# Optimization experiments

Measured on AMD Instinct MI355X. Metric: run time of the kernel, lower is better.

Reference implementation:

```python
import jax, jax.numpy as jnp
import numpy as np

S, D = 8192, 2048      # sequence length, feature dim (input_size)
H, E, K, L = 64, 64, 2, 64  # gate hidden, expert count, top-k, expert layer_size
EPS = 1e-12            # torch F.normalize eps


def setup_inputs() -> dict:
    key = jax.random.key(0)
    ks = jax.random.split(key, 5)
    x = jax.random.normal(ks[0], (S, D), dtype=jnp.float32)
    # torch nn.Linear weights have shape [out_features, in_features]
    Wg_in = jax.random.normal(ks[1], (H, D), dtype=jnp.float32) * 0.02   # gate.input
    Wg_lin = jax.random.normal(ks[2], (E, H), dtype=jnp.float32) * 0.02  # gate.linear
    Wg_out = jax.random.normal(ks[3], (1, S), dtype=jnp.float32) * 0.02  # gate.output
    We = jax.random.normal(ks[4], (E, L, D), dtype=jnp.float32) * 0.02   # expert weight bank
    return {"x": x, "Wg_in": Wg_in, "Wg_lin": Wg_lin, "Wg_out": Wg_out, "We": We}


def reference(x, Wg_in, Wg_lin, Wg_out, We):
    # --- SparseGate (eval mode: dropout = identity) ---
    h = x @ Wg_in.T                         # [S, H]
    logits = h @ Wg_lin.T                   # [S, E]
    scores = (logits.T @ Wg_out.T)[:, 0]    # Linear(S,1) applied to [E,S] -> [E]
    topv, idx = jax.lax.top_k(scores, K)    # global top-k experts for whole input
    g = jax.nn.softmax(topv)                # softmax over the k selected logits

    # --- dispatch to k selected experts (FFNN: Linear -> normalize(-1) -> GELU) ---
    Wsel = We[idx]                          # [K, L, D]
    z = jnp.einsum('sd,kld->ksl', x, Wsel)  # [K, S, L]
    z = z / jnp.maximum(jnp.linalg.norm(z, axis=-1, keepdims=True), EPS)
    z = jax.nn.gelu(z, approximate=False)   # torch GELU default is exact erf

    # --- weighted combine: sum_k g_k * expert_k(x) ---
    return jnp.einsum('k,ksl->sl', g, z)    # [S, L]
```

## Files before the change

kernel.cpp:

```cpp
#include <hip/hip_runtime.h>
#include <hip/hip_bf16.h>
#include <math.h>

#define D_DIM 2048
#define L_DIM 64
#define E_NUM 64
#define H_DIM 64

typedef float f32x4_t __attribute__((ext_vector_type(4)));
typedef __bf16 bf16x8_t __attribute__((ext_vector_type(8)));

#define WS_UPART 0u
#define WS_U     (128u * 2048u * 4u)
#define WS_V     (WS_U + 2048u * 4u)
#define WS_META  (WS_V + 256u)
#define WS_WB    (WS_META + 64u)

__global__ void k_upart(const float* __restrict__ x, const float* __restrict__ wout,
                        float* __restrict__ upart) {
  const int d4 = (blockIdx.x * 256 + threadIdx.x) * 4;
  const int s0 = blockIdx.y * 64;
  const float* xp = x + (size_t)s0 * D_DIM + d4;
  float4 acc = make_float4(0.f, 0.f, 0.f, 0.f);
#pragma unroll 8
  for (int i = 0; i < 64; ++i) {
    const float w = wout[s0 + i];
    const float4 xv = *reinterpret_cast<const float4*>(xp + (size_t)i * D_DIM);
    acc.x += xv.x * w; acc.y += xv.y * w; acc.z += xv.z * w; acc.w += xv.w * w;
  }
  *reinterpret_cast<float4*>(upart + (size_t)blockIdx.y * D_DIM + d4) = acc;
}

__global__ void k_ufinish(const float* __restrict__ upart, float* __restrict__ u) {
  const int d = blockIdx.x * 256 + threadIdx.x;
  float s = 0.f;
#pragma unroll 8
  for (int c = 0; c < 128; ++c) s += upart[(size_t)c * D_DIM + d];
  u[d] = s;
}

__global__ void k_v(const float* __restrict__ wg_in, const float* __restrict__ u,
                    float* __restrict__ v) {
  const int h = blockIdx.x;
  const int t = threadIdx.x;
  const float4* wr = reinterpret_cast<const float4*>(wg_in + (size_t)h * D_DIM);
  const float4* ur = reinterpret_cast<const float4*>(u);
  float s = 0.f;
#pragma unroll
  for (int i = t; i < 512; i += 256) {
    const float4 a = wr[i];
    const float4 b = ur[i];
    s += a.x * b.x + a.y * b.y + a.z * b.z + a.w * b.w;
  }
  __shared__ float red[4];
#pragma unroll
  for (int off = 32; off; off >>= 1) s += __shfl_down(s, off, 64);
  if ((t & 63) == 0) red[t >> 6] = s;
  __syncthreads();
  if (t == 0) v[h] = red[0] + red[1] + red[2] + red[3];
}

__global__ void k_gate(const float* __restrict__ wg_lin, const float* __restrict__ v,
                       int* __restrict__ sel, float* __restrict__ g) {
  __shared__ float vv[H_DIM];
  __shared__ float sc[E_NUM];
  const int t = threadIdx.x;
  vv[t] = v[t];
  __syncthreads();
  float s = 0.f;
#pragma unroll 8
  for (int hh = 0; hh < H_DIM; ++hh) s += wg_lin[t * H_DIM + hh] * vv[hh];
  sc[t] = s;
  __syncthreads();
  if (t == 0) {
    int b1 = 0; float m1 = sc[0];
    for (int e = 1; e < E_NUM; ++e) { if (sc[e] > m1) { m1 = sc[e]; b1 = e; } }
    int b2 = -1; float m2 = -3.4e38f;
    for (int e = 0; e < E_NUM; ++e) {
      if (e != b1 && sc[e] > m2) { m2 = sc[e]; b2 = e; }
    }
    const float e2 = expf(m2 - m1);
    const float g0 = 1.0f / (1.0f + e2);
    sel[0] = b1; sel[1] = b2;
    g[0] = g0; g[1] = 1.0f - g0;
  }
}

__global__ void k_wb(const float* __restrict__ we, const int* __restrict__ sel,
                     __hip_bfloat16* __restrict__ wb) {
  const int n = blockIdx.x;
  const int e = sel[n >> 6];
  const int l = n & 63;
  const float* src = we + ((size_t)e * L_DIM + l) * D_DIM;
  const int t = threadIdx.x;
  const float4 a = reinterpret_cast<const float4*>(src)[2 * t];
  const float4 b = reinterpret_cast<const float4*>(src)[2 * t + 1];
  union { __hip_bfloat16 h[8]; uint4 u; } pk;
  pk.h[0] = __float2bfloat16(a.x); pk.h[1] = __float2bfloat16(a.y);
  pk.h[2] = __float2bfloat16(a.z); pk.h[3] = __float2bfloat16(a.w);
  pk.h[4] = __float2bfloat16(b.x); pk.h[5] = __float2bfloat16(b.y);
  pk.h[6] = __float2bfloat16(b.z); pk.h[7] = __float2bfloat16(b.w);
  reinterpret_cast<uint4*>(wb + (size_t)n * D_DIM)[t] = pk.u;
}

__device__ __forceinline__ void async_ld16(const void* gp, void* lp) {
  __builtin_amdgcn_global_load_lds(
      (const __attribute__((address_space(1))) unsigned int*)gp,
      (__attribute__((address_space(3))) unsigned int*)lp, 16, 0, 0);
}

__device__ __forceinline__ float gelu_f(float v) {
  return 0.5f * v * (1.0f + erff(v * 0.70710678118654752440f));
}

__global__ __launch_bounds__(256) void k_moe_gemm(
    const float* __restrict__ x, const __hip_bfloat16* __restrict__ wb,
    const float* __restrict__ gw, float* __restrict__ out) {
  __shared__ __align__(16) unsigned char lds[32 * 144 + 128 * 64 * 2];
  unsigned char* ldsA0 = lds;
  unsigned char* ldsB0 = lds + 32 * 144;

  const int tid = threadIdx.x;
  const int wv = tid >> 6;
  const int lane = tid & 63;
  const int m0 = blockIdx.x * 32;
  const float g0 = gw[0], g1 = gw[1];

  const int ar = tid >> 3, ac = tid & 7;
  const float* gA = x + (size_t)(m0 + ar) * D_DIM + ac * 8;
  unsigned char* ldsAw = ldsA0 + ar * 144 + ac * 16;

  const int fr = lane & 15, fq = lane >> 4;

  f32x4_t acc00 = {0.f, 0.f, 0.f, 0.f};
  f32x4_t acc01 = acc00, acc10 = acc00, acc11 = acc00;

  for (int kk = 0; kk < D_DIM / 64; ++kk) {
    const int k0 = kk * 64;
    if (kk) __syncthreads();
    const float4 a0 = *reinterpret_cast<const float4*>(gA + k0);
    const float4 a1 = *reinterpret_cast<const float4*>(gA + k0 + 4);
    union { __hip_bfloat16 h[8]; uint4 u; } pk;
    pk.h[0] = __float2bfloat16(a0.x); pk.h[1] = __float2bfloat16(a0.y);
    pk.h[2] = __float2bfloat16(a0.z); pk.h[3] = __float2bfloat16(a0.w);
    pk.h[4] = __float2bfloat16(a1.x); pk.h[5] = __float2bfloat16(a1.y);
    pk.h[6] = __float2bfloat16(a1.z); pk.h[7] = __float2bfloat16(a1.w);
    *reinterpret_cast<uint4*>(ldsAw) = pk.u;
#pragma unroll
    for (int i = 0; i < 4; ++i) {
      const int c = i * 256 + tid;
      const int r = c >> 3, p = c & 7;
      const int kc = p ^ (r & 7);
      async_ld16(wb + (size_t)r * D_DIM + k0 + kc * 8, ldsB0 + c * 16);
    }
    __syncthreads();
    union fragu { uint4 u; bf16x8_t v; };
    fragu af[2][2], bfr[2][2];
#pragma unroll
    for (int mt = 0; mt < 2; ++mt)
#pragma unroll
      for (int ks = 0; ks < 2; ++ks)
        af[mt][ks].u = *reinterpret_cast<const uint4*>(
            ldsA0 + (mt * 16 + fr) * 144 + ks * 64 + fq * 16);
#pragma unroll
    for (int nt = 0; nt < 2; ++nt)
#pragma unroll
      for (int ks = 0; ks < 2; ++ks) {
        const int r = wv * 32 + nt * 16 + fr;
        const int kg = ks * 4 + fq;
        bfr[nt][ks].u = *reinterpret_cast<const uint4*>(
            ldsB0 + r * 128 + ((kg ^ (r & 7)) * 16));
      }
    acc00 = __builtin_amdgcn_mfma_f32_16x16x32_bf16(af[0][0].v, bfr[0][0].v, acc00, 0, 0, 0);
    acc00 = __builtin_amdgcn_mfma_f32_16x16x32_bf16(af[0][1].v, bfr[0][1].v, acc00, 0, 0, 0);
    acc01 = __builtin_amdgcn_mfma_f32_16x16x32_bf16(af[0][0].v, bfr[1][0].v, acc01, 0, 0, 0);
    acc01 = __builtin_amdgcn_mfma_f32_16x16x32_bf16(af[0][1].v, bfr[1][1].v, acc01, 0, 0, 0);
    acc10 = __builtin_amdgcn_mfma_f32_16x16x32_bf16(af[1][0].v, bfr[0][0].v, acc10, 0, 0, 0);
    acc10 = __builtin_amdgcn_mfma_f32_16x16x32_bf16(af[1][1].v, bfr[0][1].v, acc10, 0, 0, 0);
    acc11 = __builtin_amdgcn_mfma_f32_16x16x32_bf16(af[1][0].v, bfr[1][0].v, acc11, 0, 0, 0);
    acc11 = __builtin_amdgcn_mfma_f32_16x16x32_bf16(af[1][1].v, bfr[1][1].v, acc11, 0, 0, 0);
  }
  __syncthreads();
  float* z = reinterpret_cast<float*>(lds);
  {
    const int colbase = wv * 32 + fr;
#pragma unroll
    for (int reg = 0; reg < 4; ++reg) {
      const int r0 = fq * 4 + reg;
      z[r0 * 132 + colbase]             = acc00[reg];
      z[r0 * 132 + colbase + 16]        = acc01[reg];
      z[(16 + r0) * 132 + colbase]      = acc10[reg];
      z[(16 + r0) * 132 + colbase + 16] = acc11[reg];
    }
  }
  __syncthreads();
  float* ps = reinterpret_cast<float*>(lds + 16896);
  {
    const int r = tid >> 3, seg = tid & 7;
    float s = 0.f;
#pragma unroll
    for (int i2 = 0; i2 < 16; ++i2) {
      const float t2 = z[r * 132 + seg * 16 + i2];
      s += t2 * t2;
    }
    ps[r * 8 + seg] = s;
  }
  __syncthreads();
  {
    const int r = tid >> 3, j = tid & 7;
    const float s0 = ps[r * 8 + 0] + ps[r * 8 + 1] + ps[r * 8 + 2] + ps[r * 8 + 3];
    const float s1 = ps[r * 8 + 4] + ps[r * 8 + 5] + ps[r * 8 + 6] + ps[r * 8 + 7];
    const float i0 = 1.0f / fmaxf(sqrtf(s0), 1e-12f);
    const float i1 = 1.0f / fmaxf(sqrtf(s1), 1e-12f);
    float o[8];
#pragma unroll
    for (int i2 = 0; i2 < 8; ++i2) {
      const int c = j * 8 + i2;
      const float za = z[r * 132 + c] * i0;
      const float zb = z[r * 132 + 64 + c] * i1;
      o[i2] = g0 * gelu_f(za) + g1 * gelu_f(zb);
    }
    float4* op = reinterpret_cast<float4*>(out + (size_t)(m0 + r) * 64 + j * 8);
    op[0] = make_float4(o[0], o[1], o[2], o[3]);
    op[1] = make_float4(o[4], o[5], o[6], o[7]);
  }
}

extern "C" void kernel_launch(void* const* d_in, const int* in_sizes, int n_in,
                              void* d_out, int out_size, void* d_ws, size_t ws_size,
                              hipStream_t stream) {
  (void)in_sizes; (void)n_in; (void)out_size; (void)ws_size;
  const float* x      = (const float*)d_in[0];
  const float* wg_in  = (const float*)d_in[1];
  const float* wg_lin = (const float*)d_in[2];
  const float* wg_out = (const float*)d_in[3];
  const float* we     = (const float*)d_in[4];
  float* out = (float*)d_out;
  char* ws = (char*)d_ws;

  float* upart = (float*)(ws + WS_UPART);
  float* u     = (float*)(ws + WS_U);
  float* v     = (float*)(ws + WS_V);
  int*   sel   = (int*)(ws + WS_META);
  float* g     = (float*)(ws + WS_META + 8);
  __hip_bfloat16* wb = (__hip_bfloat16*)(ws + WS_WB);

  k_upart  <<<dim3(2, 128), 256, 0, stream>>>(x, wg_out, upart);
  k_ufinish<<<8, 256, 0, stream>>>(upart, u);
  k_v      <<<64, 256, 0, stream>>>(wg_in, u, v);
  k_gate   <<<1, 64, 0, stream>>>(wg_lin, v, sel, g);
  k_wb     <<<128, 256, 0, stream>>>(we, sel, wb);
  k_moe_gemm<<<256, 256, 0, stream>>>(x, wb, g, out);
}
```

Measured before the change: 167.9 us.

## Fuse gate kernels, double-buffer MoE GEMM loads, halve row tile

The three small gate kernels (u finish, v projection, expert scoring/top-k) merge into one 1024-thread block, removing launches and global round-trips. k_upart now uses 128 rows per block with two accumulators, so there are half as many partials. The expert GEMM moves to 16-row tiles with 512 blocks and double-buffers both the async B loads and the A register prefetch, overlapping loads with MFMA. The tradeoffs are lower per-block MFMA reuse, serialized partial sums in a single block, and more register and LDS use.

New measurement: 170.8 us. No clear change (+1.7%).

```diff
diff --git a/kernel.cpp b/kernel.cpp
--- a/kernel.cpp
+++ b/kernel.cpp
@@ -11,74 +11,71 @@
 typedef __bf16 bf16x8_t __attribute__((ext_vector_type(8)));
 
 #define WS_UPART 0u
-#define WS_U     (128u * 2048u * 4u)
-#define WS_V     (WS_U + 2048u * 4u)
-#define WS_META  (WS_V + 256u)
+#define WS_META  (128u * 2048u * 4u + 2048u * 4u + 256u)
 #define WS_WB    (WS_META + 64u)
 
-__global__ void k_upart(const float* __restrict__ x, const float* __restrict__ wout,
-                        float* __restrict__ upart) {
+__global__ __launch_bounds__(256) void k_upart(const float* __restrict__ x,
+                                               const float* __restrict__ wout,
+                                               float* __restrict__ upart) {
   const int d4 = (blockIdx.x * 256 + threadIdx.x) * 4;
-  const int s0 = blockIdx.y * 64;
+  const int s0 = blockIdx.y * 128;
   const float* xp = x + (size_t)s0 * D_DIM + d4;
-  float4 acc = make_float4(0.f, 0.f, 0.f, 0.f);
+  float4 acc0 = make_float4(0.f, 0.f, 0.f, 0.f);
+  float4 acc1 = make_float4(0.f, 0.f, 0.f, 0.f);
 #pragma unroll 8
-  for (int i = 0; i < 64; ++i) {
-    const float w = wout[s0 + i];
-    const float4 xv = *reinterpret_cast<const float4*>(xp + (size_t)i * D_DIM);
-    acc.x += xv.x * w; acc.y += xv.y * w; acc.z += xv.z * w; acc.w += xv.w * w;
-  }
-  *reinterpret_cast<float4*>(upart + (size_t)blockIdx.y * D_DIM + d4) = acc;
-}
-
-__global__ void k_ufinish(const float* __restrict__ upart, float* __restrict__ u) {
-  const int d = blockIdx.x * 256 + threadIdx.x;
-  float s = 0.f;
+  for (int i = 0; i < 128; i += 2) {
+    const float w0 = wout[s0 + i];
+    const float w1 = wout[s0 + i + 1];
+    const float4 a = *reinterpret_cast<const float4*>(xp + (size_t)i * D_DIM);
+    const float4 b = *reinterpret_cast<const float4*>(xp + (size_t)(i + 1) * D_DIM);
+    acc0.x += a.x * w0; acc0.y += a.y * w0; acc0.z += a.z * w0; acc0.w += a.w * w0;
+    acc1.x += b.x * w1; acc1.y += b.y * w1; acc1.z += b.z * w1; acc1.w += b.w * w1;
+  }
+  acc0.x += acc1.x; acc0.y += acc1.y; acc0.z += acc1.z; acc0.w += acc1.w;
+  *reinterpret_cast<float4*>(upart + (size_t)blockIdx.y * D_DIM + d4) = acc0;
+}
+
+__global__ __launch_bounds__(1024) void k_gate_all(
+    const float* __restrict__ upart, const float* __restrict__ wg_in,
+    const float* __restrict__ wg_lin, int* __restrict__ sel, float* __restrict__ g) {
+  __shared__ float uS[D_DIM];
+  __shared__ float vS[H_DIM];
+  __shared__ float scS[E_NUM];
+  const int t = threadIdx.x;
+  for (int dd = t; dd < D_DIM; dd += 1024) {
+    float s = 0.f;
 #pragma unroll 8
-  for (int c = 0; c < 128; ++c) s += upart[(size_t)c * D_DIM + d];
-  u[d] = s;
-}
-
-__global__ void k_v(const float* __restrict__ wg_in, const float* __restrict__ u,
-                    float* __restrict__ v) {
-  const int h = blockIdx.x;
-  const int t = threadIdx.x;
-  const float4* wr = reinterpret_cast<const float4*>(wg_in + (size_t)h * D_DIM);
-  const float4* ur = reinterpret_cast<const float4*>(u);
-  float s = 0.f;
-#pragma unroll
-  for (int i = t; i < 512; i += 256) {
-    const float4 a = wr[i];
-    const float4 b = ur[i];
-    s += a.x * b.x + a.y * b.y + a.z * b.z + a.w * b.w;
-  }
-  __shared__ float red[4];
-#pragma unroll
-  for (int off = 32; off; off >>= 1) s += __shfl_down(s, off, 64);
-  if ((t & 63) == 0) red[t >> 6] = s;
-  __syncthreads();
-  if (t == 0) v[h] = red[0] + red[1] + red[2] + red[3];
-}
-
-__global__ void k_gate(const float* __restrict__ wg_lin, const float* __restrict__ v,
-                       int* __restrict__ sel, float* __restrict__ g) {
-  __shared__ float vv[H_DIM];
-  __shared__ float sc[E_NUM];
-  const int t = threadIdx.x;
-  vv[t] = v[t];
-  __syncthreads();
-  float s = 0.f;
+    for (int c = 0; c < 64; ++c) s += upart[(size_t)c * D_DIM + dd];
+    uS[dd] = s;
+  }
+  __syncthreads();
+  const int w = t >> 6, lane = t & 63;
+  for (int hh = w; hh < H_DIM; hh += 16) {
+    const float4* wr = reinterpret_cast<const float4*>(wg_in + (size_t)hh * D_DIM);
+    float s = 0.f;
+#pragma unroll
+    for (int j = 0; j < 8; ++j) {
+      const float4 a = wr[lane + 64 * j];
+      const float* ub = &uS[(lane + 64 * j) * 4];
+      s += a.x * ub[0] + a.y * ub[1] + a.z * ub[2] + a.w * ub[3];
+    }
+#pragma unroll
+    for (int off = 32; off; off >>= 1) s += __shfl_down(s, off, 64);
+    if (lane == 0) vS[hh] = s;
+  }
+  __syncthreads();
+  if (t < E_NUM) {
+    float s = 0.f;
 #pragma unroll 8
-  for (int hh = 0; hh < H_DIM; ++hh) s += wg_lin[t * H_DIM + hh] * vv[hh];
-  sc[t] = s;
+    for (int hh = 0; hh < H_DIM; ++hh) s += wg_lin[t * H_DIM + hh] * vS[hh];
+    scS[t] = s;
+  }
   __syncthreads();
   if (t == 0) {
-    int b1 = 0; float m1 = sc[0];
-    for (int e = 1; e < E_NUM; ++e) { if (sc[e] > m1) { m1 = sc[e]; b1 = e; } }
+    int b1 = 0; float m1 = scS[0];
+    for (int e = 1; e < E_NUM; ++e) { if (scS[e] > m1) { m1 = scS[e]; b1 = e; } }
     int b2 = -1; float m2 = -3.4e38f;
-    for (int e = 0; e < E_NUM; ++e) {
-      if (e != b1 && sc[e] > m2) { m2 = sc[e]; b2 = e; }
-    }
+    for (int e = 0; e < E_NUM; ++e) { if (e != b1 && scS[e] > m2) { m2 = scS[e]; b2 = e; } }
     const float e2 = expf(m2 - m1);
     const float g0 = 1.0f / (1.0f + e2);
     sel[0] = b1; sel[1] = b2;
@@ -86,8 +83,9 @@
   }
 }
 
-__global__ void k_wb(const float* __restrict__ we, const int* __restrict__ sel,
-                     __hip_bfloat16* __restrict__ wb) {
+__global__ __launch_bounds__(256) void k_wb(const float* __restrict__ we,
+                                            const int* __restrict__ sel,
+                                            __hip_bfloat16* __restrict__ wb) {
   const int n = blockIdx.x;
   const int e = sel[n >> 6];
   const int l = n & 63;
@@ -113,55 +111,70 @@
   return 0.5f * v * (1.0f + erff(v * 0.70710678118654752440f));
 }
 
+#define A_OFF 0
+#define B_OFF 4608
+#define A_STRIDE 2304
+#define B_STRIDE 16384
 __global__ __launch_bounds__(256) void k_moe_gemm(
     const float* __restrict__ x, const __hip_bfloat16* __restrict__ wb,
     const float* __restrict__ gw, float* __restrict__ out) {
-  __shared__ __align__(16) unsigned char lds[32 * 144 + 128 * 64 * 2];
-  unsigned char* ldsA0 = lds;
-  unsigned char* ldsB0 = lds + 32 * 144;
+  __shared__ __align__(16) unsigned char lds[2 * 16 * 144 + 2 * 128 * 128];
 
   const int tid = threadIdx.x;
   const int wv = tid >> 6;
   const int lane = tid & 63;
-  const int m0 = blockIdx.x * 32;
+  const int m0 = blockIdx.x * 16;
   const float g0 = gw[0], g1 = gw[1];
 
-  const int ar = tid >> 3, ac = tid & 7;
-  const float* gA = x + (size_t)(m0 + ar) * D_DIM + ac * 8;
-  unsigned char* ldsAw = ldsA0 + ar * 144 + ac * 16;
+  const int ar = tid >> 4, ac = tid & 15;
+  const float* gA = x + (size_t)(m0 + ar) * D_DIM + ac * 4;
 
   const int fr = lane & 15, fq = lane >> 4;
 
-  f32x4_t acc00 = {0.f, 0.f, 0.f, 0.f};
-  f32x4_t acc01 = acc00, acc10 = acc00, acc11 = acc00;
-
-  for (int kk = 0; kk < D_DIM / 64; ++kk) {
-    const int k0 = kk * 64;
-    if (kk) __syncthreads();
-    const float4 a0 = *reinterpret_cast<const float4*>(gA + k0);
-    const float4 a1 = *reinterpret_cast<const float4*>(gA + k0 + 4);
-    union { __hip_bfloat16 h[8]; uint4 u; } pk;
-    pk.h[0] = __float2bfloat16(a0.x); pk.h[1] = __float2bfloat16(a0.y);
-    pk.h[2] = __float2bfloat16(a0.z); pk.h[3] = __float2bfloat16(a0.w);
-    pk.h[4] = __float2bfloat16(a1.x); pk.h[5] = __float2bfloat16(a1.y);
-    pk.h[6] = __float2bfloat16(a1.z); pk.h[7] = __float2bfloat16(a1.w);
-    *reinterpret_cast<uint4*>(ldsAw) = pk.u;
-#pragma unroll
-    for (int i = 0; i < 4; ++i) {
-      const int c = i * 256 + tid;
-      const int r = c >> 3, p = c & 7;
-      const int kc = p ^ (r & 7);
-      async_ld16(wb + (size_t)r * D_DIM + k0 + kc * 8, ldsB0 + c * 16);
-    }
-    __syncthreads();
+  f32x4_t acc0 = {0.f, 0.f, 0.f, 0.f};
+  f32x4_t acc1 = acc0;
+
+#define ISSUE_B(kk, bufo)                                                     \
+  {                                                                           \
+    const int k0_ = (kk) * 64;                                                \
+    _Pragma("unroll") for (int i_ = 0; i_ < 4; ++i_) {                        \
+      const int c_ = i_ * 256 + tid;                                          \
+      const int r_ = c_ >> 3, p_ = c_ & 7;                                    \
+      const int kc_ = p_ ^ (r_ & 7);                                          \
+      async_ld16(wb + (size_t)r_ * D_DIM + k0_ + kc_ * 8,                     \
+                 lds + B_OFF + (bufo) + c_ * 16);                             \
+    }                                                                         \
+  }
+#define WRITE_A(av, bufo)                                                     \
+  {                                                                           \
+    union { __hip_bfloat16 h[4]; uint2 u; } pk_;                              \
+    pk_.h[0] = __float2bfloat16((av).x); pk_.h[1] = __float2bfloat16((av).y); \
+    pk_.h[2] = __float2bfloat16((av).z); pk_.h[3] = __float2bfloat16((av).w); \
+    *reinterpret_cast<uint2*>(lds + A_OFF + (bufo) + ar * 144 + ac * 8) = pk_.u; \
+  }
+
+  ISSUE_B(0, 0);
+  {
+    const float4 a0 = *reinterpret_cast<const float4*>(gA);
+    WRITE_A(a0, 0);
+  }
+  __syncthreads();
+
+  for (int kk = 0; kk < 32; ++kk) {
+    const int curA = (kk & 1) * A_STRIDE, nxtA = ((kk & 1) ^ 1) * A_STRIDE;
+    const int curB = (kk & 1) * B_STRIDE, nxtB = ((kk & 1) ^ 1) * B_STRIDE;
+    float4 aN = make_float4(0.f, 0.f, 0.f, 0.f);
+    const bool more = (kk + 1) < 32;
+    if (more) {
+      ISSUE_B(kk + 1, nxtB);
+      aN = *reinterpret_cast<const float4*>(gA + (kk + 1) * 64);
+    }
     union fragu { uint4 u; bf16x8_t v; };
-    fragu af[2][2], bfr[2][2];
-#pragma unroll
-    for (int mt = 0; mt < 2; ++mt)
-#pragma unroll
-      for (int ks = 0; ks < 2; ++ks)
-        af[mt][ks].u = *reinterpret_cast<const uint4*>(
-            ldsA0 + (mt * 16 + fr) * 144 + ks * 64 + fq * 16);
+    fragu af[2], bfr[2][2];
+#pragma unroll
+    for (int ks = 0; ks < 2; ++ks)
+      af[ks].u = *reinterpret_cast<const uint4*>(
+          lds + A_OFF + curA + fr * 144 + ks * 64 + fq * 16);
 #pragma unroll
     for (int nt = 0; nt < 2; ++nt)
 #pragma unroll
@@ -169,61 +182,57 @@
         const int r = wv * 32 + nt * 16 + fr;
         const int kg = ks * 4 + fq;
         bfr[nt][ks].u = *reinterpret_cast<const uint4*>(
-            ldsB0 + r * 128 + ((kg ^ (r & 7)) * 16));
+            lds + B_OFF + curB + r * 128 + ((kg ^ (r & 7)) * 16));
       }
-    acc00 = __builtin_amdgcn_mfma_f32_16x16x32_bf16(af[0][0].v, bfr[0][0].v, acc00, 0, 0, 0);
-    acc00 = __builtin_amdgcn_mfma_f32_16x16x32_bf16(af[0][1].v, bfr[0][1].v, acc00, 0, 0, 0);
-    acc01 = __builtin_amdgcn_mfma_f32_16x16x32_bf16(af[0][0].v, bfr[1][0].v, acc01, 0, 0, 0);
-    acc01 = __builtin_amdgcn_mfma_f32_16x16x32_bf16(af[0][1].v, bfr[1][1].v, acc01, 0, 0, 0);
-    acc10 = __builtin_amdgcn_mfma_f32_16x16x32_bf16(af[1][0].v, bfr[0][0].v, acc10, 0, 0, 0);
-    acc10 = __builtin_amdgcn_mfma_f32_16x16x32_bf16(af[1][1].v, bfr[0][1].v, acc10, 0, 0, 0);
-    acc11 = __builtin_amdgcn_mfma_f32_16x16x32_bf16(af[1][0].v, bfr[1][0].v, acc11, 0, 0, 0);
-    acc11 = __builtin_amdgcn_mfma_f32_16x16x32_bf16(af[1][1].v, bfr[1][1].v, acc11, 0, 0, 0);
-  }
-  __syncthreads();
+    acc0 = __builtin_amdgcn_mfma_f32_16x16x32_bf16(af[0].v, bfr[0][0].v, acc0, 0, 0, 0);
+    acc0 = __builtin_amdgcn_mfma_f32_16x16x32_bf16(af[1].v, bfr[0][1].v, acc0, 0, 0, 0);
+    acc1 = __builtin_amdgcn_mfma_f32_16x16x32_bf16(af[0].v, bfr[1][0].v, acc1, 0, 0, 0);
+    acc1 = __builtin_amdgcn_mfma_f32_16x16x32_bf16(af[1].v, bfr[1][1].v, acc1, 0, 0, 0);
+    if (more) WRITE_A(aN, nxtA);
+    __syncthreads();
+  }
+
   float* z = reinterpret_cast<float*>(lds);
   {
     const int colbase = wv * 32 + fr;
 #pragma unroll
     for (int reg = 0; reg < 4; ++reg) {
       const int r0 = fq * 4 + reg;
-      z[r0 * 132 + colbase]             = acc00[reg];
-      z[r0 * 132 + colbase + 16]        = acc01[reg];
-      z[(16 + r0) * 132 + colbase]      = acc10[reg];
-      z[(16 + r0) * 132 + colbase + 16] = acc11[reg];
-    }
-  }
-  __syncthreads();
-  float* ps = reinterpret_cast<float*>(lds + 16896);
-  {
-    const int r = tid >> 3, seg = tid & 7;
-    float s = 0.f;
-#pragma unroll
-    for (int i2 = 0; i2 < 16; ++i2) {
-      const float t2 = z[r * 132 + seg * 16 + i2];
+      z[r0 * 132 + colbase]      = acc0[reg];
+      z[r0 * 132 + colbase + 16] = acc1[reg];
+    }
+  }
+  __syncthreads();
+  float* ps = reinterpret_cast<float*>(lds + 16 * 132 * 4);
+  {
+    const int r = tid >> 4, seg = tid & 15;
+    float s = 0.f;
+#pragma unroll
+    for (int i2 = 0; i2 < 8; ++i2) {
+      const float t2 = z[r * 132 + seg * 8 + i2];
       s += t2 * t2;
     }
-    ps[r * 8 + seg] = s;
-  }
-  __syncthreads();
-  {
-    const int r = tid >> 3, j = tid & 7;
-    const float s0 = ps[r * 8 + 0] + ps[r * 8 + 1] + ps[r * 8 + 2] + ps[r * 8 + 3];
-    const float s1 = ps[r * 8 + 4] + ps[r * 8 + 5] + ps[r * 8 + 6] + ps[r * 8 + 7];
+    ps[r * 16 + seg] = s;
+  }
+  __syncthreads();
+  {
+    const int r = tid >> 4, j = tid & 15;
+    float s0 = 0.f, s1 = 0.f;
+#pragma unroll
+    for (int i2 = 0; i2 < 8; ++i2) { s0 += ps[r * 16 + i2]; s1 += ps[r * 16 + 8 + i2]; }
     const float i0 = 1.0f / fmaxf(sqrtf(s0), 1e-12f);
     const float i1 = 1.0f / fmaxf(sqrtf(s1), 1e-12f);
-    float o[8];
-#pragma unroll
-    for (int i2 = 0; i2 < 8; ++i2) {
-      const int c = j * 8 + i2;
-      const float za = z[r * 132 + c] * i0;
-      const float zb = z[r * 132 + 64 + c] * i1;
-      o[i2] = g0 * gelu_f(za) + g1 * gelu_f(zb);
-    }
-    float4* op = reinterpret_cast<float4*>(out + (size_t)(m0 + r) * 64 + j * 8);
-    op[0] = make_float4(o[0], o[1], o[2], o[3]);
-    op[1] = make_float4(o[4], o[5], o[6], o[7]);
-  }
+    float o[4];
+#pragma unroll
+    for (int i2 = 0; i2 < 4; ++i2) {
+      const int c = j * 4 + i2;
+      o[i2] = g0 * gelu_f(z[r * 132 + c] * i0) + g1 * gelu_f(z[r * 132 + 64 + c] * i1);
+    }
+    *reinterpret_cast<float4*>(out + (size_t)(m0 + r) * 64 + j * 4) =
+        make_float4(o[0], o[1], o[2], o[3]);
+  }
+#undef ISSUE_B
+#undef WRITE_A
 }
 
 extern "C" void kernel_launch(void* const* d_in, const int* in_sizes, int n_in,
@@ -239,16 +248,12 @@
   char* ws = (char*)d_ws;
 
   float* upart = (float*)(ws + WS_UPART);
-  float* u     = (float*)(ws + WS_U);
-  float* v     = (float*)(ws + WS_V);
   int*   sel   = (int*)(ws + WS_META);
   float* g     = (float*)(ws + WS_META + 8);
   __hip_bfloat16* wb = (__hip_bfloat16*)(ws + WS_WB);
 
-  k_upart  <<<dim3(2, 128), 256, 0, stream>>>(x, wg_out, upart);
-  k_ufinish<<<8, 256, 0, stream>>>(upart, u);
-  k_v      <<<64, 256, 0, stream>>>(wg_in, u, v);
-  k_gate   <<<1, 64, 0, stream>>>(wg_lin, v, sel, g);
-  k_wb     <<<128, 256, 0, stream>>>(we, sel, wb);
-  k_moe_gemm<<<256, 256, 0, stream>>>(x, wb, g, out);
-}
+  k_upart   <<<dim3(2, 64), 256, 0, stream>>>(x, wg_out, upart);
+  k_gate_all<<<1, 1024, 0, stream>>>(upart, wg_in, wg_lin, sel, g);
+  k_wb      <<<128, 256, 0, stream>>>(we, sel, wb);
+  k_moe_gemm<<<512, 256, 0, stream>>>(x, wb, g, out);
+}
```
